# Kernel tuning notes

Measured on AMD Instinct MI355X. Metric: run time of the kernel, lower is better.

The kernel has to match this reference:

```python
import math
import jax, jax.numpy as jnp
import numpy as np

NQ, NK = 4096, 8192
D_Q, D_K, D_ATTN, H, D_OUT = 256, 256, 64, 4, 256


def setup_inputs() -> dict:
    key = jax.random.key(0)
    ks = jax.random.split(key, 10)
    s = 0.02
    return {
        "x_Q": jax.random.normal(ks[0], (NQ, D_Q), jnp.float32),
        "x_K": jax.random.normal(ks[1], (NK, D_K), jnp.float32),
        "mask": jax.random.randint(ks[2], (NQ, NK), 0, 2, jnp.int32),
        # per-head projection weights, stored as (H, in, out) so y = x @ W
        "Wq": jax.random.normal(ks[3], (H, D_Q, D_ATTN), jnp.float32) * s,
        "Wk": jax.random.normal(ks[4], (H, D_K, D_ATTN), jnp.float32) * s,
        "Wv": jax.random.normal(ks[5], (H, D_K, D_ATTN), jnp.float32) * s,
        # per-head gate: Linear(d_Q, 1) + sigmoid
        "Wg": jax.random.normal(ks[6], (H, D_Q), jnp.float32) * s,
        "bg": jax.random.normal(ks[7], (H,), jnp.float32) * s,
        # output projection Linear(d_attn, d_out) with bias
        "Wo": jax.random.normal(ks[8], (D_ATTN, D_OUT), jnp.float32) * s,
        "bo": jax.random.normal(ks[9], (D_OUT,), jnp.float32) * s,
    }


def reference(x_Q, x_K, mask, Wq, Wk, Wv, Wg, bg, Wo, bo):
    m = mask.astype(x_Q.dtype)  # (NQ, NK) 0/1
    # Stacked per-head projections (original loops over heads)
    Q = jnp.einsum("nq,hqa->hna", x_Q, Wq)  # (H, NQ, A)
    K = jnp.einsum("mk,hka->hma", x_K, Wk)  # (H, NK, A)
    V = jnp.einsum("mk,hka->hma", x_K, Wv)  # (H, NK, A)
    scale = 1.0 / math.sqrt(D_ATTN)
    scores = jnp.einsum("hna,hma->hnm", Q, K) * scale  # (H, NQ, NK)
    # masked_softmax: (mask * x).masked_fill(mask == 0, -inf) then softmax over keys
    X = jnp.where(m == 0, -jnp.inf, m * scores)
    attn = jax.nn.softmax(X, axis=-1)
    heads = jnp.einsum("hnm,hma->hna", attn, V)  # (H, NQ, A)
    gates = jax.nn.sigmoid(jnp.einsum("nq,hq->hn", x_Q, Wg) + bg[:, None])  # (H, NQ)
    combined = jnp.einsum("hna,hn->na", heads, gates)  # (NQ, A)
    return combined @ Wo + bo  # (NQ, D_OUT)
```

## Files before the change

### kernel.cpp

```cpp
#include <hip/hip_runtime.h>

#define NQ 4096
#define NK 8192
#define DQK 256
#define DA 64
#define NH 4
#define DOUT 256
#define KSPLIT 16
#define KLEN (NK / KSPLIT)
#define NQT (NQ / 32)
#define LOG2E 1.44269504088896340736f
#define QSCALE (0.125f * LOG2E)

typedef __attribute__((ext_vector_type(8))) short bf16x8;
typedef __attribute__((ext_vector_type(4))) float f32x4;
typedef __attribute__((ext_vector_type(4))) _Float16 f16x4;

__device__ inline unsigned short f2bf(float f) {
  union { float f; unsigned u; } v; v.f = f;
  unsigned r = v.u + 0x7fff + ((v.u >> 16) & 1);
  return (unsigned short)(r >> 16);
}

__global__ __launch_bounds__(256) void maskbits_kernel(
    const int* __restrict__ mask, unsigned long long* __restrict__ bits64) {
  const int NW = 4096 * 4;
  int wid = blockIdx.x * 4 + (threadIdx.x >> 6);
  int lane = threadIdx.x & 63;
  for (int j = 0; j < 8; ++j) {
    int v[4];
#pragma unroll
    for (int u = 0; u < 4; ++u) {
      int c = wid + (j * 4 + u) * NW;
      v[u] = mask[(size_t)(c >> 7) * NK + (c & 127) * 64 + lane];
    }
#pragma unroll
    for (int u = 0; u < 4; ++u) {
      unsigned long long b = __ballot(v[u] != 0);
      int c = wid + (j * 4 + u) * NW;
      if (lane == 0) bits64[c] = b;
    }
  }
}

__global__ __launch_bounds__(256) void proj_kernel(
    const float* __restrict__ xQ, const float* __restrict__ xK,
    const float* __restrict__ Wq, const float* __restrict__ Wk,
    const float* __restrict__ Wv,
    unsigned short* __restrict__ Qp, unsigned short* __restrict__ Kp,
    unsigned short* __restrict__ Vt) {
  __shared__ __align__(16) unsigned short Wt[64][264];

  int b = blockIdx.x;
  int proj, h, rb;
  if (b < 64)        { proj = 0; h = b >> 4;  rb = b & 15; }
  else if (b < 192)  { proj = 1; b -= 64;  h = b >> 5; rb = b & 31; }
  else               { proj = 2; b -= 192; h = b >> 5; rb = b & 31; }
  const float* x = (proj == 0) ? xQ : xK;
  const float* W = (proj == 0 ? Wq : (proj == 1 ? Wk : Wv)) + (size_t)h * 256 * 64;

  for (int i = threadIdx.x; i < 16384; i += 256)
    Wt[i & 63][i >> 6] = f2bf(W[i]);
  __syncthreads();

  int lane = threadIdx.x & 63, wv = threadIdx.x >> 6;
  int quad = lane >> 4, n16 = lane & 15;
  int r0 = rb * 256 + wv * 64;

  f32x4 acc[4][4];
#pragma unroll
  for (int mt = 0; mt < 4; ++mt)
#pragma unroll
    for (int nt = 0; nt < 4; ++nt)
      acc[mt][nt] = (f32x4){0.f, 0.f, 0.f, 0.f};

#pragma unroll
  for (int it = 0; it < 8; ++it) {
    const int k0 = it * 32;
    bf16x8 af[4];
#pragma unroll
    for (int mt = 0; mt < 4; ++mt) {
      const float* xp = x + (size_t)(r0 + mt * 16 + n16) * 256 + k0 + quad * 8;
      const float4 a0 = *(const float4*)xp;
      const float4 a1 = *(const float4*)(xp + 4);
      bf16x8 a;
      a[0] = (short)f2bf(a0.x); a[1] = (short)f2bf(a0.y);
      a[2] = (short)f2bf(a0.z); a[3] = (short)f2bf(a0.w);
      a[4] = (short)f2bf(a1.x); a[5] = (short)f2bf(a1.y);
      a[6] = (short)f2bf(a1.z); a[7] = (short)f2bf(a1.w);
      af[mt] = a;
    }
    bf16x8 bfr[4];
#pragma unroll
    for (int nt = 0; nt < 4; ++nt)
      bfr[nt] = *(const bf16x8*)&Wt[nt * 16 + n16][k0 + quad * 8];
#pragma unroll
    for (int mt = 0; mt < 4; ++mt)
#pragma unroll
      for (int nt = 0; nt < 4; ++nt)
        acc[mt][nt] = __builtin_amdgcn_mfma_f32_16x16x32_bf16(
            af[mt], bfr[nt], acc[mt][nt], 0, 0, 0);
  }

  if (proj < 2) {
    unsigned short* outp =
        (proj == 0 ? Qp : Kp) + (size_t)h * (size_t)(proj == 0 ? NQ : NK) * 64;
    const float sc = (proj == 0) ? QSCALE : 1.0f;
#pragma unroll
    for (int mt = 0; mt < 4; ++mt)
#pragma unroll
      for (int nt = 0; nt < 4; ++nt)
#pragma unroll
        for (int r = 0; r < 4; ++r) {
          int row = r0 + mt * 16 + quad * 4 + r;
          int col = nt * 16 + n16;
          outp[(size_t)row * 64 + col] = f2bf(acc[mt][nt][r] * sc);
        }
  } else {
    unsigned short* vtp = Vt + (size_t)h * 64 * NK;
#pragma unroll
    for (int mt = 0; mt < 4; ++mt)
#pragma unroll
      for (int nt = 0; nt < 4; ++nt) {
        int d = nt * 16 + n16;
        int key0 = r0 + mt * 16 + quad * 4;
        ushort4 pk;
        pk.x = f2bf(acc[mt][nt][0]); pk.y = f2bf(acc[mt][nt][1]);
        pk.z = f2bf(acc[mt][nt][2]); pk.w = f2bf(acc[mt][nt][3]);
        *(ushort4*)&vtp[(size_t)d * NK + key0] = pk;
      }
  }
}

__global__ void gates_kernel(const float* __restrict__ xQ,
                             const float* __restrict__ Wg,
                             const float* __restrict__ bg,
                             float* __restrict__ gates) {
  int gid = blockIdx.x * 256 + threadIdx.x;
  int n = gid >> 6;
  int lane = threadIdx.x & 63;
  float4 xv = *(const float4*)(xQ + (size_t)n * 256 + lane * 4);
  float p[NH];
#pragma unroll
  for (int h = 0; h < NH; ++h) {
    float4 wv = *(const float4*)(Wg + h * 256 + lane * 4);
    p[h] = xv.x * wv.x + xv.y * wv.y + xv.z * wv.z + xv.w * wv.w;
  }
#pragma unroll
  for (int off = 32; off >= 1; off >>= 1)
#pragma unroll
    for (int h = 0; h < NH; ++h) p[h] += __shfl_xor(p[h], off);
  if (lane == 0) {
#pragma unroll
    for (int h = 0; h < NH; ++h)
      gates[(size_t)h * NQ + n] = 1.f / (1.f + __expf(-(p[h] + bg[h])));
  }
}

__global__ __launch_bounds__(256) void attn_kernel(
    const unsigned short* __restrict__ Qp, const unsigned short* __restrict__ Kp,
    const unsigned short* __restrict__ Vt, const unsigned* __restrict__ bits,
    _Float16* __restrict__ Opart, float* __restrict__ Lpart) {
  __shared__ __align__(16) unsigned short Plds[4][32][40];

  int b = blockIdx.x;
  int ks = b & 15, h = (b >> 4) & 3, qg = b >> 6;
  int wv = threadIdx.x >> 6, lane = threadIdx.x & 63;
  int quad = lane >> 4, n16 = lane & 15;
  int qt = qg * 4 + wv;
  int qb = qt * 32;

  bf16x8 qf[2][2];
#pragma unroll
  for (int qc = 0; qc < 2; ++qc)
#pragma unroll
    for (int c = 0; c < 2; ++c)
      qf[qc][c] = *(const bf16x8*)&Qp[((size_t)h * NQ + qb + qc * 16 + n16) * 64 +
                                      c * 32 + quad * 8];

  bf16x8 onesA;
  {
    short v = (n16 == 0) ? (short)0x3F80 : (short)0;
#pragma unroll
    for (int i = 0; i < 8; ++i) onesA[i] = v;
  }

  f32x4 o[4][2];
#pragma unroll
  for (int dt = 0; dt < 4; ++dt)
#pragma unroll
    for (int qc = 0; qc < 2; ++qc) o[dt][qc] = (f32x4){0.f, 0.f, 0.f, 0.f};
  f32x4 l5[2];
  l5[0] = (f32x4){0.f, 0.f, 0.f, 0.f};
  l5[1] = (f32x4){0.f, 0.f, 0.f, 0.f};

  const unsigned short* Kptr =
      Kp + (size_t)h * NK * 64 + (size_t)(ks * KLEN + n16) * 64 + quad * 8;
  const unsigned short* Vptr =
      Vt + (size_t)h * 64 * NK + (size_t)n16 * NK + ks * KLEN + quad * 8;
  const unsigned* bq0 = bits + (size_t)(qb + n16) * (NK / 32) + ks * (KLEN / 32);
  const unsigned* bq1 = bits + (size_t)(qb + 16 + n16) * (NK / 32) + ks * (KLEN / 32);

  for (int kb = 0; kb < KLEN / 32; ++kb) {
    unsigned wqa0 = bq0[kb];
    unsigned wqa1 = bq1[kb];

    bf16x8 kf[2][2];
#pragma unroll
    for (int kr = 0; kr < 2; ++kr)
#pragma unroll
      for (int c = 0; c < 2; ++c)
        kf[kr][c] = *(const bf16x8*)(Kptr + kr * 16 * 64 + c * 32);

    bf16x8 vfr[4];
#pragma unroll
    for (int dt = 0; dt < 4; ++dt)
      vfr[dt] = *(const bf16x8*)(Vptr + (size_t)dt * 16 * NK);

    f32x4 s[2][2];
#pragma unroll
    for (int kr = 0; kr < 2; ++kr)
#pragma unroll
      for (int qc = 0; qc < 2; ++qc) {
        f32x4 acc = (f32x4){0.f, 0.f, 0.f, 0.f};
        acc = __builtin_amdgcn_mfma_f32_16x16x32_bf16(kf[kr][0], qf[qc][0], acc, 0, 0, 0);
        acc = __builtin_amdgcn_mfma_f32_16x16x32_bf16(kf[kr][1], qf[qc][1], acc, 0, 0, 0);
        s[kr][qc] = acc;
      }

#pragma unroll
    for (int qc = 0; qc < 2; ++qc) {
      unsigned wq0 = (qc == 0 ? wqa0 : wqa1) >> (quad * 4);
      unsigned rp[8];
#pragma unroll
      for (int kr = 0; kr < 2; ++kr)
#pragma unroll
        for (int r = 0; r < 4; ++r) {
          float e = __builtin_amdgcn_exp2f(s[kr][qc][r]);
          unsigned pe = __float_as_uint(e);
          pe = (wq0 & (1u << (kr * 16 + r))) ? pe : 0u;
          rp[kr * 4 + r] = pe + 0x8000u;
        }
      uint2 w01, w23;
      w01.x = __builtin_amdgcn_perm(rp[1], rp[0], 0x07060302u);
      w01.y = __builtin_amdgcn_perm(rp[3], rp[2], 0x07060302u);
      w23.x = __builtin_amdgcn_perm(rp[5], rp[4], 0x07060302u);
      w23.y = __builtin_amdgcn_perm(rp[7], rp[6], 0x07060302u);
      unsigned short* prow = &Plds[wv][qc * 16 + n16][0];
      *(uint2*)(prow + quad * 4) = w01;
      *(uint2*)(prow + 16 + quad * 4) = w23;
    }

    bf16x8 pb0 = *(const bf16x8*)&Plds[wv][n16][quad * 8];
    bf16x8 pb1 = *(const bf16x8*)&Plds[wv][16 + n16][quad * 8];

#pragma unroll
    for (int dt = 0; dt < 4; ++dt) {
      o[dt][0] = __builtin_amdgcn_mfma_f32_16x16x32_bf16(vfr[dt], pb0, o[dt][0], 0, 0, 0);
      o[dt][1] = __builtin_amdgcn_mfma_f32_16x16x32_bf16(vfr[dt], pb1, o[dt][1], 0, 0, 0);
    }
    l5[0] = __builtin_amdgcn_mfma_f32_16x16x32_bf16(onesA, pb0, l5[0], 0, 0, 0);
    l5[1] = __builtin_amdgcn_mfma_f32_16x16x32_bf16(onesA, pb1, l5[1], 0, 0, 0);

    Kptr += 32 * 64;
    Vptr += 32;
  }

  const size_t tb = ((size_t)h * NQT + qt) * KSPLIT + ks;
#pragma unroll
  for (int qc = 0; qc < 2; ++qc) {
#pragma unroll
    for (int dt = 0; dt < 4; ++dt) {
      size_t idx = (tb * 32 + qc * 16 + n16) * 64 + dt * 16 + quad * 4;
      f16x4 ov;
      ov[0] = (_Float16)o[dt][qc][0]; ov[1] = (_Float16)o[dt][qc][1];
      ov[2] = (_Float16)o[dt][qc][2]; ov[3] = (_Float16)o[dt][qc][3];
      *(f16x4*)&Opart[idx] = ov;
    }
  }
  if (quad == 0) {
    Lpart[tb * 32 + n16] = l5[0][0];
    Lpart[tb * 32 + 16 + n16] = l5[1][0];
  }
}

__global__ __launch_bounds__(256) void combine_kernel(
    const _Float16* __restrict__ Opart, const float* __restrict__ Lpart,
    const float* __restrict__ gates, const float* __restrict__ Wo,
    const float* __restrict__ bo, float* __restrict__ out) {
  __shared__ float comb[16][64];
  int nb = blockIdx.x;
  int tid = threadIdx.x;
  int r4 = tid >> 6, a = tid & 63;
  int qt = nb >> 1, rbase = (nb & 1) * 16;

  for (int p = 0; p < 4; ++p) {
    int r = p * 4 + r4;
    int rl = rbase + r;
    int n = nb * 16 + r;
    float csum = 0.f;
#pragma unroll
    for (int h = 0; h < NH; ++h) {
      size_t t0 = ((size_t)h * NQT + qt) * KSPLIT;
      float accO = 0.f, lt = 0.f;
#pragma unroll
      for (int s = 0; s < KSPLIT; ++s) {
        size_t t = t0 + s;
        accO += (float)Opart[(t * 32 + rl) * 64 + a];
        lt += Lpart[t * 32 + rl];
      }
      csum += gates[(size_t)h * NQ + n] * accO / lt;
    }
    comb[r][a] = csum;
  }
  __syncthreads();

  int j = tid;
  float accv[16];
#pragma unroll
  for (int r = 0; r < 16; ++r) accv[r] = bo[j];
  for (int aa = 0; aa < 64; ++aa) {
    float w = Wo[(size_t)aa * 256 + j];
#pragma unroll
    for (int r = 0; r < 16; ++r) accv[r] = fmaf(comb[r][aa], w, accv[r]);
  }
#pragma unroll
  for (int r = 0; r < 16; ++r)
    out[(size_t)(nb * 16 + r) * 256 + j] = accv[r];
}

extern "C" void kernel_launch(void* const* d_in, const int* in_sizes, int n_in,
                              void* d_out, int out_size, void* d_ws, size_t ws_size,
                              hipStream_t stream) {
  const float* xQ  = (const float*)d_in[0];
  const float* xK  = (const float*)d_in[1];
  const int*   mask= (const int*)d_in[2];
  const float* Wq  = (const float*)d_in[3];
  const float* Wk  = (const float*)d_in[4];
  const float* Wv  = (const float*)d_in[5];
  const float* Wg  = (const float*)d_in[6];
  const float* bg  = (const float*)d_in[7];
  const float* Wo  = (const float*)d_in[8];
  const float* bo  = (const float*)d_in[9];
  float* out = (float*)d_out;

  char* ws = (char*)d_ws;
  unsigned short* Qp   = (unsigned short*)(ws + 0);
  unsigned short* Kp   = (unsigned short*)(ws + 2097152);
  unsigned short* Vt   = (unsigned short*)(ws + 6291456);
  unsigned*       bits = (unsigned*)(ws + 10485760);
  float*          gts  = (float*)(ws + 14680064);
  float*          Lp   = (float*)(ws + 14745600);
  _Float16*       Op   = (_Float16*)(ws + 15794176);

  maskbits_kernel<<<dim3(4096), dim3(256), 0, stream>>>(
      mask, (unsigned long long*)bits);
  proj_kernel<<<dim3(320), dim3(256), 0, stream>>>(xQ, xK, Wq, Wk, Wv, Qp, Kp, Vt);
  gates_kernel<<<dim3(NQ / 4), dim3(256), 0, stream>>>(xQ, Wg, bg, gts);
  attn_kernel<<<dim3(2048), dim3(256), 0, stream>>>(Qp, Kp, Vt, bits, Op, Lp);
  combine_kernel<<<dim3(NQ / 16), dim3(256), 0, stream>>>(Op, Lp, gts, Wo, bo, out);
}
```

Before: 446.2 us.

## Prefetch K/V registers in attention, fuse gates into combine, retune maskbits grid

The attention loop now software-pipelines K and V fragment loads one iteration ahead and double-buffers the per-wave P tile in LDS. P conversion switches from a manual bit trick to the packed bf16 conversion intrinsic. The separate gates kernel is removed and its computation is folded into the combine kernel via a small shared-memory reduction. The maskbits kernel launches twice as many blocks with more loads in flight per thread. Prefetching raises register pressure and may lower occupancy in the attention kernel.

```diff
diff --git a/kernel.cpp b/kernel.cpp
--- a/kernel.cpp
+++ b/kernel.cpp
@@ -1,4 +1,5 @@
 #include <hip/hip_runtime.h>
+#include <hip/hip_bf16.h>
 
 #define NQ 4096
 #define NK 8192
@@ -22,22 +23,28 @@
   return (unsigned short)(r >> 16);
 }
 
+__device__ inline unsigned pk2(float a, float b) {
+  float2 t; t.x = a; t.y = b;
+  __hip_bfloat162 r = __float22bfloat162_rn(t);
+  return *(unsigned*)&r;
+}
+
 __global__ __launch_bounds__(256) void maskbits_kernel(
     const int* __restrict__ mask, unsigned long long* __restrict__ bits64) {
-  const int NW = 4096 * 4;
+  const int NW = 8192 * 4;
   int wid = blockIdx.x * 4 + (threadIdx.x >> 6);
   int lane = threadIdx.x & 63;
-  for (int j = 0; j < 8; ++j) {
-    int v[4];
-#pragma unroll
-    for (int u = 0; u < 4; ++u) {
-      int c = wid + (j * 4 + u) * NW;
+  for (int j = 0; j < 2; ++j) {
+    int v[8];
+#pragma unroll
+    for (int u = 0; u < 8; ++u) {
+      int c = wid + (j * 8 + u) * NW;
       v[u] = mask[(size_t)(c >> 7) * NK + (c & 127) * 64 + lane];
     }
 #pragma unroll
-    for (int u = 0; u < 4; ++u) {
+    for (int u = 0; u < 8; ++u) {
       unsigned long long b = __ballot(v[u] != 0);
-      int c = wid + (j * 4 + u) * NW;
+      int c = wid + (j * 8 + u) * NW;
       if (lane == 0) bits64[c] = b;
     }
   }
@@ -132,36 +139,11 @@
   }
 }
 
-__global__ void gates_kernel(const float* __restrict__ xQ,
-                             const float* __restrict__ Wg,
-                             const float* __restrict__ bg,
-                             float* __restrict__ gates) {
-  int gid = blockIdx.x * 256 + threadIdx.x;
-  int n = gid >> 6;
-  int lane = threadIdx.x & 63;
-  float4 xv = *(const float4*)(xQ + (size_t)n * 256 + lane * 4);
-  float p[NH];
-#pragma unroll
-  for (int h = 0; h < NH; ++h) {
-    float4 wv = *(const float4*)(Wg + h * 256 + lane * 4);
-    p[h] = xv.x * wv.x + xv.y * wv.y + xv.z * wv.z + xv.w * wv.w;
-  }
-#pragma unroll
-  for (int off = 32; off >= 1; off >>= 1)
-#pragma unroll
-    for (int h = 0; h < NH; ++h) p[h] += __shfl_xor(p[h], off);
-  if (lane == 0) {
-#pragma unroll
-    for (int h = 0; h < NH; ++h)
-      gates[(size_t)h * NQ + n] = 1.f / (1.f + __expf(-(p[h] + bg[h])));
-  }
-}
-
 __global__ __launch_bounds__(256) void attn_kernel(
     const unsigned short* __restrict__ Qp, const unsigned short* __restrict__ Kp,
     const unsigned short* __restrict__ Vt, const unsigned* __restrict__ bits,
     _Float16* __restrict__ Opart, float* __restrict__ Lpart) {
-  __shared__ __align__(16) unsigned short Plds[4][32][40];
+  __shared__ __align__(16) unsigned short Plds[4][2][32][40];
 
   int b = blockIdx.x;
   int ks = b & 15, h = (b >> 4) & 3, qg = b >> 6;
@@ -201,21 +183,33 @@
   const unsigned* bq0 = bits + (size_t)(qb + n16) * (NK / 32) + ks * (KLEN / 32);
   const unsigned* bq1 = bits + (size_t)(qb + 16 + n16) * (NK / 32) + ks * (KLEN / 32);
 
+  bf16x8 kf[2][2], vf[4];
+#pragma unroll
+  for (int kr = 0; kr < 2; ++kr)
+#pragma unroll
+    for (int c = 0; c < 2; ++c)
+      kf[kr][c] = *(const bf16x8*)(Kptr + kr * 16 * 64 + c * 32);
+#pragma unroll
+  for (int dt = 0; dt < 4; ++dt)
+    vf[dt] = *(const bf16x8*)(Vptr + (size_t)dt * 16 * NK);
+
+#pragma unroll
   for (int kb = 0; kb < KLEN / 32; ++kb) {
+    bf16x8 kn[2][2], vn[4];
+    if (kb < KLEN / 32 - 1) {
+      const unsigned short* Kn = Kptr + (size_t)(kb + 1) * 32 * 64;
+      const unsigned short* Vn = Vptr + (kb + 1) * 32;
+#pragma unroll
+      for (int kr = 0; kr < 2; ++kr)
+#pragma unroll
+        for (int c = 0; c < 2; ++c)
+          kn[kr][c] = *(const bf16x8*)(Kn + kr * 16 * 64 + c * 32);
+#pragma unroll
+      for (int dt = 0; dt < 4; ++dt)
+        vn[dt] = *(const bf16x8*)(Vn + (size_t)dt * 16 * NK);
+    }
     unsigned wqa0 = bq0[kb];
     unsigned wqa1 = bq1[kb];
-
-    bf16x8 kf[2][2];
-#pragma unroll
-    for (int kr = 0; kr < 2; ++kr)
-#pragma unroll
-      for (int c = 0; c < 2; ++c)
-        kf[kr][c] = *(const bf16x8*)(Kptr + kr * 16 * 64 + c * 32);
-
-    bf16x8 vfr[4];
-#pragma unroll
-    for (int dt = 0; dt < 4; ++dt)
-      vfr[dt] = *(const bf16x8*)(Vptr + (size_t)dt * 16 * NK);
 
     f32x4 s[2][2];
 #pragma unroll
@@ -228,42 +222,45 @@
         s[kr][qc] = acc;
       }
 
+    unsigned short* pbuf = &Plds[wv][kb & 1][0][0];
 #pragma unroll
     for (int qc = 0; qc < 2; ++qc) {
       unsigned wq0 = (qc == 0 ? wqa0 : wqa1) >> (quad * 4);
-      unsigned rp[8];
+      float e[8];
 #pragma unroll
       for (int kr = 0; kr < 2; ++kr)
 #pragma unroll
         for (int r = 0; r < 4; ++r) {
-          float e = __builtin_amdgcn_exp2f(s[kr][qc][r]);
-          unsigned pe = __float_as_uint(e);
-          pe = (wq0 & (1u << (kr * 16 + r))) ? pe : 0u;
-          rp[kr * 4 + r] = pe + 0x8000u;
+          float ev = __builtin_amdgcn_exp2f(s[kr][qc][r]);
+          e[kr * 4 + r] = (wq0 & (1u << (kr * 16 + r))) ? ev : 0.f;
         }
+      unsigned short* prow = pbuf + (qc * 16 + n16) * 40;
       uint2 w01, w23;
-      w01.x = __builtin_amdgcn_perm(rp[1], rp[0], 0x07060302u);
-      w01.y = __builtin_amdgcn_perm(rp[3], rp[2], 0x07060302u);
-      w23.x = __builtin_amdgcn_perm(rp[5], rp[4], 0x07060302u);
-      w23.y = __builtin_amdgcn_perm(rp[7], rp[6], 0x07060302u);
-      unsigned short* prow = &Plds[wv][qc * 16 + n16][0];
+      w01.x = pk2(e[0], e[1]); w01.y = pk2(e[2], e[3]);
+      w23.x = pk2(e[4], e[5]); w23.y = pk2(e[6], e[7]);
       *(uint2*)(prow + quad * 4) = w01;
       *(uint2*)(prow + 16 + quad * 4) = w23;
     }
 
-    bf16x8 pb0 = *(const bf16x8*)&Plds[wv][n16][quad * 8];
-    bf16x8 pb1 = *(const bf16x8*)&Plds[wv][16 + n16][quad * 8];
+    bf16x8 pb0 = *(const bf16x8*)(pbuf + n16 * 40 + quad * 8);
+    bf16x8 pb1 = *(const bf16x8*)(pbuf + (16 + n16) * 40 + quad * 8);
 
 #pragma unroll
     for (int dt = 0; dt < 4; ++dt) {
-      o[dt][0] = __builtin_amdgcn_mfma_f32_16x16x32_bf16(vfr[dt], pb0, o[dt][0], 0, 0, 0);
-      o[dt][1] = __builtin_amdgcn_mfma_f32_16x16x32_bf16(vfr[dt], pb1, o[dt][1], 0, 0, 0);
+      o[dt][0] = __builtin_amdgcn_mfma_f32_16x16x32_bf16(vf[dt], pb0, o[dt][0], 0, 0, 0);
+      o[dt][1] = __builtin_amdgcn_mfma_f32_16x16x32_bf16(vf[dt], pb1, o[dt][1], 0, 0, 0);
     }
     l5[0] = __builtin_amdgcn_mfma_f32_16x16x32_bf16(onesA, pb0, l5[0], 0, 0, 0);
     l5[1] = __builtin_amdgcn_mfma_f32_16x16x32_bf16(onesA, pb1, l5[1], 0, 0, 0);
 
-    Kptr += 32 * 64;
-    Vptr += 32;
+    if (kb < KLEN / 32 - 1) {
+#pragma unroll
+      for (int kr = 0; kr < 2; ++kr)
+#pragma unroll
+        for (int c = 0; c < 2; ++c) kf[kr][c] = kn[kr][c];
+#pragma unroll
+      for (int dt = 0; dt < 4; ++dt) vf[dt] = vn[dt];
+    }
   }
 
   const size_t tb = ((size_t)h * NQT + qt) * KSPLIT + ks;
@@ -286,18 +283,38 @@
 
 __global__ __launch_bounds__(256) void combine_kernel(
     const _Float16* __restrict__ Opart, const float* __restrict__ Lpart,
-    const float* __restrict__ gates, const float* __restrict__ Wo,
+    const float* __restrict__ xQ, const float* __restrict__ Wg,
+    const float* __restrict__ bg, const float* __restrict__ Wo,
     const float* __restrict__ bo, float* __restrict__ out) {
   __shared__ float comb[16][64];
+  __shared__ float gred[16][4][4];
+  __shared__ float glds[16][4];
   int nb = blockIdx.x;
   int tid = threadIdx.x;
+
+  {
+    int r = tid >> 4, hh = (tid >> 2) & 3, c = tid & 3;
+    const float* xp = xQ + (size_t)(nb * 16 + r) * 256 + c * 64;
+    const float* wp = Wg + hh * 256 + c * 64;
+    float s = 0.f;
+#pragma unroll
+    for (int e = 0; e < 64; ++e) s = fmaf(xp[e], wp[e], s);
+    gred[r][hh][c] = s;
+  }
+  __syncthreads();
+  if (tid < 64) {
+    int r = tid >> 2, hh = tid & 3;
+    float s = gred[r][hh][0] + gred[r][hh][1] + gred[r][hh][2] + gred[r][hh][3];
+    glds[r][hh] = 1.f / (1.f + __expf(-(s + bg[hh])));
+  }
+  __syncthreads();
+
   int r4 = tid >> 6, a = tid & 63;
   int qt = nb >> 1, rbase = (nb & 1) * 16;
 
   for (int p = 0; p < 4; ++p) {
     int r = p * 4 + r4;
     int rl = rbase + r;
-    int n = nb * 16 + r;
     float csum = 0.f;
 #pragma unroll
     for (int h = 0; h < NH; ++h) {
@@ -309,7 +326,7 @@
         accO += (float)Opart[(t * 32 + rl) * 64 + a];
         lt += Lpart[t * 32 + rl];
       }
-      csum += gates[(size_t)h * NQ + n] * accO / lt;
+      csum += glds[r][h] * accO / lt;
     }
     comb[r][a] = csum;
   }
@@ -349,14 +366,13 @@
   unsigned short* Kp   = (unsigned short*)(ws + 2097152);
   unsigned short* Vt   = (unsigned short*)(ws + 6291456);
   unsigned*       bits = (unsigned*)(ws + 10485760);
-  float*          gts  = (float*)(ws + 14680064);
   float*          Lp   = (float*)(ws + 14745600);
   _Float16*       Op   = (_Float16*)(ws + 15794176);
 
-  maskbits_kernel<<<dim3(4096), dim3(256), 0, stream>>>(
+  maskbits_kernel<<<dim3(8192), dim3(256), 0, stream>>>(
       mask, (unsigned long long*)bits);
   proj_kernel<<<dim3(320), dim3(256), 0, stream>>>(xQ, xK, Wq, Wk, Wv, Qp, Kp, Vt);
-  gates_kernel<<<dim3(NQ / 4), dim3(256), 0, stream>>>(xQ, Wg, bg, gts);
   attn_kernel<<<dim3(2048), dim3(256), 0, stream>>>(Qp, Kp, Vt, bits, Op, Lp);
-  combine_kernel<<<dim3(NQ / 16), dim3(256), 0, stream>>>(Op, Lp, gts, Wo, bo, out);
-}
+  combine_kernel<<<dim3(NQ / 16), dim3(256), 0, stream>>>(Op, Lp, xQ, Wg, bg,
+                                                          Wo, bo, out);
+}
```

Result: faster. 429.5 us (-3.7%).
